# Kernel tuning notes

Measured on AMD Instinct MI355X. Metric: run time of the kernel, lower is better.

The kernel has to match this reference:

```python
import jax, jax.numpy as jnp
import numpy as np

B, I, H = 4096, 1024, 1024

def setup_inputs() -> dict:
    key = jax.random.key(0)
    ks = jax.random.split(key, 10)
    return {
        "input": jax.random.normal(ks[0], (B, I), dtype=jnp.float32),
        "hx": jax.random.normal(ks[1], (B, H), dtype=jnp.float32),
        "cx": jax.random.normal(ks[2], (B, H), dtype=jnp.float32),
        "noise_q": jax.random.uniform(ks[3], (1,), dtype=jnp.float32),
        "noise_e": jax.random.uniform(ks[4], (1,), dtype=jnp.float32),
        "weight_ih": jax.random.normal(ks[5], (4 * H, I), dtype=jnp.float32),
        "weight_hh": jax.random.normal(ks[6], (4 * H, H), dtype=jnp.float32),
        "bias_ih": jax.random.normal(ks[7], (4 * H,), dtype=jnp.float32),
        "bias_hh": jax.random.normal(ks[8], (4 * H,), dtype=jnp.float32),
        # pre-drawn standard-normal noise (torch.randn in the original forward)
        "eps_c": jax.random.normal(jax.random.fold_in(key, 101), (B, H), dtype=jnp.float32),
        "eps_h": jax.random.normal(jax.random.fold_in(key, 102), (B, H), dtype=jnp.float32),
    }

def reference(input, hx, cx, noise_q, noise_e, weight_ih, weight_hh, bias_ih, bias_hh, eps_c, eps_h):
    # gates: [B, 4H]
    gates = input @ weight_ih.T + bias_ih + hx @ weight_hh.T + bias_hh
    ingate, forgetgate, cellgate, outgate = jnp.split(gates, 4, axis=1)
    ingate = jax.nn.sigmoid(ingate)
    forgetgate = jax.nn.sigmoid(forgetgate)
    cellgate = jnp.tanh(cellgate)
    outgate = jax.nn.sigmoid(outgate)
    cy = forgetgate * cx + ingate * cellgate + jnp.sqrt(noise_e) * eps_c
    hy = outgate * jnp.tanh(cy) + jnp.sqrt(noise_q) * eps_h
    return (hy, cy)
```

## Files before the change

kernel.cpp:

```cpp
#include <hip/hip_runtime.h>
#include <hip/hip_bf16.h>
#include <cstdint>
#include <cstddef>


#define B_ROWS 4096
#define HDIM   1024
#define KDIM   2048
#define BM     256
#define T_STEPS 64

typedef unsigned short u16;
using f32x4  = __attribute__((ext_vector_type(4))) float;
using short8 = __attribute__((ext_vector_type(8))) short;
using half8  = __attribute__((ext_vector_type(8))) _Float16;

__device__ __forceinline__ u16 f2h_bits(float f) {
    _Float16 h = (_Float16)f;
    return __builtin_bit_cast(u16, h);
}

__global__ void pack_kernel(const float* __restrict__ input, const float* __restrict__ hx,
                            const float* __restrict__ wih, const float* __restrict__ whh,
                            u16* __restrict__ Ap, u16* __restrict__ Wp)
{
    const int NA = 16 * 2 * 64 * 8 * 64;
    const int NW = 16 * 4 * 64 * 4 * 64;
    int stride = gridDim.x * blockDim.x;
    for (int i = blockIdx.x * blockDim.x + threadIdx.x; i < NA + NW; i += stride) {
        int isW = (i >= NA) ? 1 : 0;
        int e = isW ? i - NA : i;
        int lane = e & 63;
        int fr = lane & 15, fk = lane >> 4;
        int kt = isW ? ((e >> 8) & 63) : ((e >> 9) & 63);
        int k  = kt * 32 + fk * 8;
        int row;
        if (isW) {
            int g  = (e >> 6) & 3;
            int wn = (e >> 14) & 3;
            int hqq = e >> 16;
            row = g * 1024 + hqq * 64 + wn * 16 + fr;
        } else {
            int m  = (e >> 6) & 7;
            int wmm = (e >> 15) & 1;
            int mii = e >> 16;
            row = mii * 256 + wmm * 128 + m * 16 + fr;
        }
        const float* s0 = isW ? wih : input;
        const float* s1 = isW ? whh : hx;
        const float* src = (k < 1024) ? (s0 + (size_t)row * 1024 + k)
                                      : (s1 + (size_t)row * 1024 + (k - 1024));
        float4 v0 = *(const float4*)src;
        float4 v1 = *(const float4*)(src + 4);
        u16* dst = (isW ? Wp : Ap) + (size_t)e * 8;
        *(ushort4*)dst = make_ushort4(f2h_bits(v0.x), f2h_bits(v0.y),
                                      f2h_bits(v0.z), f2h_bits(v0.w));
        *(ushort4*)(dst + 4) = make_ushort4(f2h_bits(v1.x), f2h_bits(v1.y),
                                            f2h_bits(v1.z), f2h_bits(v1.w));
    }
}

__device__ __forceinline__ float sigmf(float x) { return 1.0f / (1.0f + __expf(-x)); }
__device__ __forceinline__ float tanhfast(float x) { return 1.0f - 2.0f / (1.0f + __expf(2.0f * x)); }

__launch_bounds__(512, 1)
__global__ void lstm_fused(const u16* __restrict__ Ap, const u16* __restrict__ Wp,
                           const float* __restrict__ cx, const float* __restrict__ eps_c,
                           const float* __restrict__ eps_h,
                           const float* __restrict__ bias_ih, const float* __restrict__ bias_hh,
                           const float* __restrict__ noise_q, const float* __restrict__ noise_e,
                           float* __restrict__ out)
{
    int bid = blockIdx.x;
    int w = (bid & 7) * 32 + (bid >> 3);
    int mi = w & 15;
    int hq = w >> 4;
    int bm0 = mi * BM;
    int h0 = hq * 64;

    int tid  = threadIdx.x;
    int lane = tid & 63;
    int wid  = tid >> 6;
    int wm   = wid >> 2;
    int wn   = wid & 3;
    int fr   = lane & 15, fk = lane >> 4;

    const u16* pA = Ap + ((size_t)(mi * 2 + wm)) * (64 * 8 * 64 * 8) + lane * 8;
    const u16* pW = Wp + ((size_t)(hq * 4 + wn)) * (64 * 4 * 64 * 8) + lane * 8;

#define LD8(p) __builtin_bit_cast(half8, *(const short8*)(p))

#define LOADF(AA, WW, kt) do { \
        _Pragma("unroll") \
        for (int m = 0; m < 8; ++m) AA[m] = LD8(pA + (size_t)(kt) * 4096 + m * 512); \
        _Pragma("unroll") \
        for (int g = 0; g < 4; ++g) WW[g] = LD8(pW + (size_t)(kt) * 2048 + g * 512); \
    } while (0)

#define DOMFMA(AA, WW) do { \
        __builtin_amdgcn_s_setprio(1); \
        _Pragma("unroll") \
        for (int g = 0; g < 4; ++g) \
            _Pragma("unroll") \
            for (int m = 0; m < 8; ++m) \
                acc[m][g] = __builtin_amdgcn_mfma_f32_16x16x32_f16(AA[m], WW[g], acc[m][g], 0, 0, 0); \
        __builtin_amdgcn_s_setprio(0); \
    } while (0)

    f32x4 acc[8][4];
#pragma unroll
    for (int m = 0; m < 8; ++m)
#pragma unroll
        for (int g = 0; g < 4; ++g)
            acc[m][g] = (f32x4){0.f, 0.f, 0.f, 0.f};

    half8 aX[8], wX[4], aY[8], wY[4];
    LOADF(aX, wX, 0);

#pragma unroll 1
    for (int t = 0; t < T_STEPS; t += 2) {
        LOADF(aY, wY, t + 1);
        DOMFMA(aX, wX);
        if (t + 2 < T_STEPS) LOADF(aX, wX, t + 2);
        DOMFMA(aY, wY);
    }

    float sq_e = sqrtf(noise_e[0]);
    float sq_q = sqrtf(noise_q[0]);
    int h = h0 + wn * 16 + fr;
    float bsum[4];
#pragma unroll
    for (int g = 0; g < 4; ++g)
        bsum[g] = bias_ih[g * 1024 + h] + bias_hh[g * 1024 + h];
#pragma unroll
    for (int m = 0; m < 8; ++m) {
        int r0 = bm0 + wm * 128 + m * 16 + fk * 4;
#pragma unroll
        for (int j = 0; j < 4; ++j) {
            int r = r0 + j;
            float gi = acc[m][0][j] + bsum[0];
            float gf = acc[m][1][j] + bsum[1];
            float gc = acc[m][2][j] + bsum[2];
            float go = acc[m][3][j] + bsum[3];
            float ig = sigmf(gi), fg = sigmf(gf);
            float cg = tanhfast(gc), og = sigmf(go);
            size_t off = (size_t)r * HDIM + h;
            float cyv = fg * cx[off] + ig * cg + sq_e * eps_c[off];
            float hyv = og * tanhfast(cyv) + sq_q * eps_h[off];
            out[off] = hyv;
            out[(size_t)B_ROWS * HDIM + off] = cyv;
        }
    }
}

extern "C" void kernel_launch(void* const* d_in, const int* in_sizes, int n_in,
                              void* d_out, int out_size, void* d_ws, size_t ws_size,
                              hipStream_t stream)
{
    const float* input = (const float*)d_in[0];
    const float* hx    = (const float*)d_in[1];
    const float* cx    = (const float*)d_in[2];
    const float* nq    = (const float*)d_in[3];
    const float* ne    = (const float*)d_in[4];
    const float* wih   = (const float*)d_in[5];
    const float* whh   = (const float*)d_in[6];
    const float* bih   = (const float*)d_in[7];
    const float* bhh   = (const float*)d_in[8];
    const float* epsc  = (const float*)d_in[9];
    const float* epsh  = (const float*)d_in[10];
    float* out = (float*)d_out;

    u16* Ap = (u16*)d_ws;
    u16* Wp = Ap + (size_t)B_ROWS * KDIM;

    hipLaunchKernelGGL(pack_kernel, dim3(2048), dim3(256), 0, stream,
                       input, hx, wih, whh, Ap, Wp);
    hipLaunchKernelGGL(lstm_fused, dim3(256), dim3(512), 0, stream,
                       Ap, Wp, cx, epsc, epsh, bih, bhh, nq, ne, out);
}
```

Before: 101.1 us.

## Enlarge per-wave tile to 128x32 with 4 waves per block

Each block now runs 4 waves instead of 8, and each wave computes a 128-row by 32-column (x4 gates) tile, holding an 8x8 grid of MFMA accumulators. The pack kernel's weight layout is changed to match, interleaving two 16-column sub-tiles per gate. This raises arithmetic intensity per wave and cuts redundant A-fragment loads across waves. In exchange, accumulator register use doubles (256 VGPRs for acc plus 32 fragment registers), which risks spilling or low latency hiding with fewer waves per CU.

Result: slower. 185.0 us (+83.0%).

```diff
diff --git a/kernel.cpp b/kernel.cpp
--- a/kernel.cpp
+++ b/kernel.cpp
@@ -25,23 +25,23 @@
                             u16* __restrict__ Ap, u16* __restrict__ Wp)
 {
     const int NA = 16 * 2 * 64 * 8 * 64;
-    const int NW = 16 * 4 * 64 * 4 * 64;
+    const int NW = 16 * 2 * 64 * 8 * 64;
     int stride = gridDim.x * blockDim.x;
     for (int i = blockIdx.x * blockDim.x + threadIdx.x; i < NA + NW; i += stride) {
         int isW = (i >= NA) ? 1 : 0;
         int e = isW ? i - NA : i;
         int lane = e & 63;
         int fr = lane & 15, fk = lane >> 4;
-        int kt = isW ? ((e >> 8) & 63) : ((e >> 9) & 63);
+        int kt = (e >> 9) & 63;
         int k  = kt * 32 + fk * 8;
         int row;
         if (isW) {
-            int g  = (e >> 6) & 3;
-            int wn = (e >> 14) & 3;
+            int nn  = (e >> 6) & 7;
+            int wnn = (e >> 15) & 1;
             int hqq = e >> 16;
-            row = g * 1024 + hqq * 64 + wn * 16 + fr;
+            row = (nn >> 1) * 1024 + hqq * 64 + wnn * 32 + (nn & 1) * 16 + fr;
         } else {
-            int m  = (e >> 6) & 7;
+            int m   = (e >> 6) & 7;
             int wmm = (e >> 15) & 1;
             int mii = e >> 16;
             row = mii * 256 + wmm * 128 + m * 16 + fr;
@@ -63,7 +63,7 @@
 __device__ __forceinline__ float sigmf(float x) { return 1.0f / (1.0f + __expf(-x)); }
 __device__ __forceinline__ float tanhfast(float x) { return 1.0f - 2.0f / (1.0f + __expf(2.0f * x)); }
 
-__launch_bounds__(512, 1)
+__launch_bounds__(256, 1)
 __global__ void lstm_fused(const u16* __restrict__ Ap, const u16* __restrict__ Wp,
                            const float* __restrict__ cx, const float* __restrict__ eps_c,
                            const float* __restrict__ eps_h,
@@ -81,12 +81,12 @@
     int tid  = threadIdx.x;
     int lane = tid & 63;
     int wid  = tid >> 6;
-    int wm   = wid >> 2;
-    int wn   = wid & 3;
+    int wm   = wid >> 1;
+    int wn   = wid & 1;
     int fr   = lane & 15, fk = lane >> 4;
 
-    const u16* pA = Ap + ((size_t)(mi * 2 + wm)) * (64 * 8 * 64 * 8) + lane * 8;
-    const u16* pW = Wp + ((size_t)(hq * 4 + wn)) * (64 * 4 * 64 * 8) + lane * 8;
+    const u16* pA = Ap + (size_t)(mi * 2 + wm) * 262144 + lane * 8;
+    const u16* pW = Wp + (size_t)(hq * 2 + wn) * 262144 + lane * 8;
 
 #define LD8(p) __builtin_bit_cast(half8, *(const short8*)(p))
 
@@ -94,27 +94,27 @@
         _Pragma("unroll") \
         for (int m = 0; m < 8; ++m) AA[m] = LD8(pA + (size_t)(kt) * 4096 + m * 512); \
         _Pragma("unroll") \
-        for (int g = 0; g < 4; ++g) WW[g] = LD8(pW + (size_t)(kt) * 2048 + g * 512); \
+        for (int n = 0; n < 8; ++n) WW[n] = LD8(pW + (size_t)(kt) * 4096 + n * 512); \
     } while (0)
 
 #define DOMFMA(AA, WW) do { \
         __builtin_amdgcn_s_setprio(1); \
         _Pragma("unroll") \
-        for (int g = 0; g < 4; ++g) \
+        for (int n = 0; n < 8; ++n) \
             _Pragma("unroll") \
             for (int m = 0; m < 8; ++m) \
-                acc[m][g] = __builtin_amdgcn_mfma_f32_16x16x32_f16(AA[m], WW[g], acc[m][g], 0, 0, 0); \
+                acc[m][n] = __builtin_amdgcn_mfma_f32_16x16x32_f16(AA[m], WW[n], acc[m][n], 0, 0, 0); \
         __builtin_amdgcn_s_setprio(0); \
     } while (0)
 
-    f32x4 acc[8][4];
+    f32x4 acc[8][8];
 #pragma unroll
     for (int m = 0; m < 8; ++m)
 #pragma unroll
-        for (int g = 0; g < 4; ++g)
-            acc[m][g] = (f32x4){0.f, 0.f, 0.f, 0.f};
+        for (int n = 0; n < 8; ++n)
+            acc[m][n] = (f32x4){0.f, 0.f, 0.f, 0.f};
 
-    half8 aX[8], wX[4], aY[8], wY[4];
+    half8 aX[8], wX[8], aY[8], wY[8];
     LOADF(aX, wX, 0);
 
 #pragma unroll 1
@@ -127,28 +127,32 @@
 
     float sq_e = sqrtf(noise_e[0]);
     float sq_q = sqrtf(noise_q[0]);
-    int h = h0 + wn * 16 + fr;
-    float bsum[4];
+    int hbase = h0 + wn * 32 + fr;
 #pragma unroll
-    for (int g = 0; g < 4; ++g)
-        bsum[g] = bias_ih[g * 1024 + h] + bias_hh[g * 1024 + h];
+    for (int hh = 0; hh < 2; ++hh) {
+        int h = hbase + hh * 16;
+        float bsum[4];
 #pragma unroll
-    for (int m = 0; m < 8; ++m) {
-        int r0 = bm0 + wm * 128 + m * 16 + fk * 4;
+        for (int g = 0; g < 4; ++g)
+            bsum[g] = bias_ih[g * 1024 + h] + bias_hh[g * 1024 + h];
 #pragma unroll
-        for (int j = 0; j < 4; ++j) {
-            int r = r0 + j;
-            float gi = acc[m][0][j] + bsum[0];
-            float gf = acc[m][1][j] + bsum[1];
-            float gc = acc[m][2][j] + bsum[2];
-            float go = acc[m][3][j] + bsum[3];
-            float ig = sigmf(gi), fg = sigmf(gf);
-            float cg = tanhfast(gc), og = sigmf(go);
-            size_t off = (size_t)r * HDIM + h;
-            float cyv = fg * cx[off] + ig * cg + sq_e * eps_c[off];
-            float hyv = og * tanhfast(cyv) + sq_q * eps_h[off];
-            out[off] = hyv;
-            out[(size_t)B_ROWS * HDIM + off] = cyv;
+        for (int m = 0; m < 8; ++m) {
+            int r0 = bm0 + wm * 128 + m * 16 + fk * 4;
+#pragma unroll
+            for (int j = 0; j < 4; ++j) {
+                int r = r0 + j;
+                float gi = acc[m][0 + hh][j] + bsum[0];
+                float gf = acc[m][2 + hh][j] + bsum[1];
+                float gc = acc[m][4 + hh][j] + bsum[2];
+                float go = acc[m][6 + hh][j] + bsum[3];
+                float ig = sigmf(gi), fg = sigmf(gf);
+                float cg = tanhfast(gc), og = sigmf(go);
+                size_t off = (size_t)r * HDIM + h;
+                float cyv = fg * cx[off] + ig * cg + sq_e * eps_c[off];
+                float hyv = og * tanhfast(cyv) + sq_q * eps_h[off];
+                out[off] = hyv;
+                out[(size_t)B_ROWS * HDIM + off] = cyv;
+            }
         }
     }
 }
@@ -175,6 +179,6 @@
 
     hipLaunchKernelGGL(pack_kernel, dim3(2048), dim3(256), 0, stream,
                        input, hx, wih, whh, Ap, Wp);
-    hipLaunchKernelGGL(lstm_fused, dim3(256), dim3(512), 0, stream,
+    hipLaunchKernelGGL(lstm_fused, dim3(256), dim3(256), 0, stream,
                        Ap, Wp, cx, epsc, epsh, bih, bhh, nq, ne, out);
 }
```
